# Optimization experiments

Measured on AMD Instinct MI355X. Metric: run time of the kernel, lower is better.

The kernel has to match this reference:

```python
import jax, jax.numpy as jnp
import numpy as np

N_NODES = 50000
N_EDGES = 800000
IN_DIM = 96
HID = 96


def setup_inputs() -> dict:
    key = jax.random.key(0)
    k1, k2, k3, k4 = jax.random.split(key, 4)
    x = jax.random.normal(k1, (N_NODES, IN_DIM), dtype=jnp.float32)
    edge_index = jax.random.randint(k2, (2, N_EDGES), 0, N_NODES, dtype=jnp.int64)
    s1 = 1.0 / np.sqrt(IN_DIM)
    s2 = 1.0 / np.sqrt(HID)
    W1 = jax.random.normal(k3, (IN_DIM, HID), dtype=jnp.float32) * s1
    b1 = jnp.zeros((HID,), dtype=jnp.float32)
    W2 = jax.random.normal(k4, (HID, HID), dtype=jnp.float32) * s2
    b2 = jnp.zeros((HID,), dtype=jnp.float32)
    return {"x": x, "edge_index": edge_index, "W1": W1, "b1": b1, "W2": W2, "b2": b2}


def _gcn_conv(x, src, dst, norm, W, b, n_nodes):
    # x' = D^{-1/2}(A+I)D^{-1/2} X W + b  (PyG GCNConv semantics)
    xw = x @ W                           # [N, out]
    msg = xw[src] * norm[:, None]        # gather + edge-normalize, [E+N, out]
    agg = jax.ops.segment_sum(msg, dst, num_segments=n_nodes)  # scatter-add
    return agg + b


def reference(x, edge_index, W1, b1, W2, b2):
    n_nodes = x.shape[0]
    loops = jnp.arange(n_nodes, dtype=edge_index.dtype)
    src = jnp.concatenate([edge_index[0], loops])  # sources (j)
    dst = jnp.concatenate([edge_index[1], loops])  # targets (i), aggregation index
    # symmetric normalization with self-loops; degree counted at targets
    deg = jax.ops.segment_sum(jnp.ones(dst.shape, dtype=x.dtype), dst, num_segments=n_nodes)
    dinv = jnp.where(deg > 0, jax.lax.rsqrt(deg), 0.0)
    norm = dinv[src] * dinv[dst]
    h = jax.nn.relu(_gcn_conv(x, src, dst, norm, W1, b1, n_nodes))
    h = jax.nn.relu(_gcn_conv(h, src, dst, norm, W2, b2, n_nodes))
    return h
```

## Files before the change

### kernel.cpp

```cpp
#include <hip/hip_runtime.h>

#define N_NODES 50000
#define N_EDGES 800000
#define DIM 96
#define FEAT_ELEMS (N_NODES * DIM)
#define NBLK 196

typedef __attribute__((ext_vector_type(8))) short short8;
typedef __attribute__((ext_vector_type(4))) float float4v;

__device__ __forceinline__ float bf16_to_f32(unsigned short u) {
    unsigned int w = ((unsigned int)u) << 16;
    float f;
    __builtin_memcpy(&f, &w, 4);
    return f;
}
__device__ __forceinline__ unsigned short f32_to_bf16_rne(float f) {
    unsigned int w;
    __builtin_memcpy(&w, &f, 4);
    unsigned int r = (w + 0x7FFFu + ((w >> 16) & 1u)) >> 16;
    return (unsigned short)r;
}

__device__ __forceinline__ int edge_at(const void* ep, int is64, int idx) {
    if (is64) return (int)((const long long*)ep)[idx];
    return ((const int*)ep)[idx];
}

__global__ __launch_bounds__(256) void prolog_kernel(const unsigned int* edges,
                                                     const unsigned int* x,
                                                     int* flagE, int* flagF, int* cnt) {
    __shared__ unsigned int sh[256];
    int t = threadIdx.x;
    int b = blockIdx.x;
    if (b < NBLK) {
        int i = b * 256 + t;
        if (i < N_NODES) cnt[i] = 0;
        return;
    }
    if (b == NBLK) {
        if (t < 64) {
            unsigned int acc = 0;
            for (int k = 0; k < 4; ++k) {
                int idx = t * 4 + k;
                int pos = 1 + 2 * idx * 3109;
                acc |= edges[pos];
            }
            sh[t] = acc;
        }
        __syncthreads();
        if (t == 0) {
            unsigned int a = 0;
            for (int i = 0; i < 64; ++i) a |= sh[i];
            *flagE = (a == 0u) ? 1 : 0;
        }
        return;
    }
    unsigned int w = x[t * 9000];
    unsigned int e = (w >> 7) & 0xFFu;
    sh[t] = (e >= 100u && e <= 135u) ? 1u : 0u;
    __syncthreads();
    if (t == 0) {
        int c = 0;
        for (int i = 0; i < 256; ++i) c += (int)sh[i];
        *flagF = (c >= 128) ? 1 : 0;
    }
}

__global__ __launch_bounds__(256) void count_compact_kernel(const void* edges,
                                                            const int* flagE, int* cnt,
                                                            unsigned short* srcu,
                                                            unsigned short* dstu,
                                                            unsigned short* rank) {
    int e = blockIdx.x * 256 + threadIdx.x;
    if (e >= N_EDGES) return;
    int is64 = *flagE;
    int s = edge_at(edges, is64, e);
    int d = edge_at(edges, is64, N_EDGES + e);
    srcu[e] = (unsigned short)s;
    dstu[e] = (unsigned short)d;
    rank[e] = (unsigned short)atomicAdd(&cnt[d], 1);
}

__global__ __launch_bounds__(256) void scan_blocksum_kernel(const int* cnt, int* blockSums) {
    __shared__ int sh[256];
    int i = blockIdx.x * 256 + threadIdx.x;
    sh[threadIdx.x] = (i < N_NODES) ? cnt[i] : 0;
    __syncthreads();
    for (int off = 128; off > 0; off >>= 1) {
        if (threadIdx.x < off) sh[threadIdx.x] += sh[threadIdx.x + off];
        __syncthreads();
    }
    if (threadIdx.x == 0) blockSums[blockIdx.x] = sh[0];
}

__global__ __launch_bounds__(256) void scan_offsets_kernel(const int* blockSums,
                                                           int* blockOffs, int* row_ptr) {
    __shared__ int sh[256];
    int t = threadIdx.x;
    int v = (t < NBLK) ? blockSums[t] : 0;
    sh[t] = v;
    __syncthreads();
    for (int off = 1; off < 256; off <<= 1) {
        int u = (t >= off) ? sh[t - off] : 0;
        __syncthreads();
        sh[t] += u;
        __syncthreads();
    }
    if (t < NBLK) blockOffs[t] = sh[t] - v;
    if (t == 255) row_ptr[N_NODES] = sh[255];
}

__global__ __launch_bounds__(256) void scan_apply_kernel(const int* cnt, const int* blockOffs,
                                                         int* row_ptr, float* dinv) {
    __shared__ int sh[256];
    int t = threadIdx.x;
    int i = blockIdx.x * 256 + t;
    int c = (i < N_NODES) ? cnt[i] : 0;
    sh[t] = c;
    __syncthreads();
    for (int off = 1; off < 256; off <<= 1) {
        int u = (t >= off) ? sh[t - off] : 0;
        __syncthreads();
        sh[t] += u;
        __syncthreads();
    }
    if (i < N_NODES) {
        int excl = sh[t] - c + blockOffs[blockIdx.x];
        row_ptr[i] = excl;
        dinv[i]    = rsqrtf((float)(c + 1));
    }
}

__global__ __launch_bounds__(256) void fill_direct_kernel(const unsigned short* __restrict__ dstu,
                                                          const unsigned short* __restrict__ srcu,
                                                          const unsigned short* __restrict__ rank,
                                                          const int* __restrict__ row_ptr,
                                                          unsigned short* __restrict__ csr_src) {
    int e = blockIdx.x * 256 + threadIdx.x;
    if (e >= N_EDGES) return;
    int d = dstu[e];
    int pos = row_ptr[d] + (int)rank[e];
    csr_src[pos] = srcu[e];
}

__global__ __launch_bounds__(256) void convert_kernel(const void* x, const int* flagF,
                                                      unsigned short* xb) {
    int i4 = (blockIdx.x * 256 + threadIdx.x) * 4;
    if (i4 >= FEAT_ELEMS) return;
    int isbf16 = *flagF;
    ushort4 o;
    if (isbf16) {
        o = *(const ushort4*)((const unsigned short*)x + i4);
    } else {
        float4 v = *(const float4*)((const float*)x + i4);
        o.x = f32_to_bf16_rne(v.x);
        o.y = f32_to_bf16_rne(v.y);
        o.z = f32_to_bf16_rne(v.z);
        o.w = f32_to_bf16_rne(v.w);
    }
    *(ushort4*)(xb + i4) = o;
}

__global__ __launch_bounds__(256) void gather_kernel(const unsigned short* __restrict__ feat,
                                                     const int* __restrict__ row_ptr,
                                                     const unsigned short* __restrict__ csr_src,
                                                     const float* __restrict__ dinv,
                                                     unsigned short* __restrict__ aggb) {
    int gid = blockIdx.x * 256 + threadIdx.x;
    int g = gid >> 4;
    int lane = gid & 15;
    if (g >= N_NODES) return;
    float di = dinv[g];
    int gb = g * DIM + lane * 2;
    ushort2 sv0 = *(const ushort2*)&feat[gb];
    ushort2 sv1 = *(const ushort2*)&feat[gb + 32];
    ushort2 sv2 = *(const ushort2*)&feat[gb + 64];
    float wself = di * di;
    float a0 = wself * bf16_to_f32(sv0.x), a1 = wself * bf16_to_f32(sv0.y);
    float a2 = wself * bf16_to_f32(sv1.x), a3 = wself * bf16_to_f32(sv1.y);
    float a4 = wself * bf16_to_f32(sv2.x), a5 = wself * bf16_to_f32(sv2.y);
    int e = row_ptr[g], e1 = row_ptr[g + 1];
    for (; e + 2 <= e1; e += 2) {
        int s0 = csr_src[e];
        int s1 = csr_src[e + 1];
        float w0 = dinv[s0] * di;
        float w1 = dinv[s1] * di;
        int b0 = s0 * DIM + lane * 2;
        int b1 = s1 * DIM + lane * 2;
        ushort2 p0 = *(const ushort2*)&feat[b0];
        ushort2 p1 = *(const ushort2*)&feat[b0 + 32];
        ushort2 p2 = *(const ushort2*)&feat[b0 + 64];
        ushort2 q0 = *(const ushort2*)&feat[b1];
        ushort2 q1 = *(const ushort2*)&feat[b1 + 32];
        ushort2 q2 = *(const ushort2*)&feat[b1 + 64];
        a0 = fmaf(w0, bf16_to_f32(p0.x), a0);  a1 = fmaf(w0, bf16_to_f32(p0.y), a1);
        a2 = fmaf(w0, bf16_to_f32(p1.x), a2);  a3 = fmaf(w0, bf16_to_f32(p1.y), a3);
        a4 = fmaf(w0, bf16_to_f32(p2.x), a4);  a5 = fmaf(w0, bf16_to_f32(p2.y), a5);
        a0 = fmaf(w1, bf16_to_f32(q0.x), a0);  a1 = fmaf(w1, bf16_to_f32(q0.y), a1);
        a2 = fmaf(w1, bf16_to_f32(q1.x), a2);  a3 = fmaf(w1, bf16_to_f32(q1.y), a3);
        a4 = fmaf(w1, bf16_to_f32(q2.x), a4);  a5 = fmaf(w1, bf16_to_f32(q2.y), a5);
    }
    if (e < e1) {
        int s = csr_src[e];
        float w = dinv[s] * di;
        int b0 = s * DIM + lane * 2;
        ushort2 p0 = *(const ushort2*)&feat[b0];
        ushort2 p1 = *(const ushort2*)&feat[b0 + 32];
        ushort2 p2 = *(const ushort2*)&feat[b0 + 64];
        a0 = fmaf(w, bf16_to_f32(p0.x), a0);  a1 = fmaf(w, bf16_to_f32(p0.y), a1);
        a2 = fmaf(w, bf16_to_f32(p1.x), a2);  a3 = fmaf(w, bf16_to_f32(p1.y), a3);
        a4 = fmaf(w, bf16_to_f32(p2.x), a4);  a5 = fmaf(w, bf16_to_f32(p2.y), a5);
    }
    unsigned int o0 = (unsigned int)f32_to_bf16_rne(a0) | ((unsigned int)f32_to_bf16_rne(a1) << 16);
    unsigned int o1 = (unsigned int)f32_to_bf16_rne(a2) | ((unsigned int)f32_to_bf16_rne(a3) << 16);
    unsigned int o2 = (unsigned int)f32_to_bf16_rne(a4) | ((unsigned int)f32_to_bf16_rne(a5) << 16);
    *(unsigned int*)&aggb[gb]      = o0;
    *(unsigned int*)&aggb[gb + 32] = o1;
    *(unsigned int*)&aggb[gb + 64] = o2;
}

__global__ __launch_bounds__(256) void gemm_mfma_kernel(const unsigned short* __restrict__ A,
                                                        const void* W, const void* bias,
                                                        const int* flagF,
                                                        void* out, int outMode) {
    __shared__ unsigned short Wlin[DIM * DIM];
    __shared__ unsigned short Wsw[3 * 6 * 64 * 8];
    __shared__ float bs[DIM];
    int wBf16 = *flagF;
    int outBf16 = (outMode == 2) ? wBf16 : outMode;

    if (wBf16) {
        const ushort4* W4 = (const ushort4*)W;
        ushort4* L4 = (ushort4*)Wlin;
        for (int i = threadIdx.x; i < DIM * DIM / 4; i += 256) L4[i] = W4[i];
        if (threadIdx.x < DIM)
            bs[threadIdx.x] = bf16_to_f32(((const unsigned short*)bias)[threadIdx.x]);
    } else {
        const float* Wf = (const float*)W;
        for (int i = threadIdx.x; i < DIM * DIM; i += 256) Wlin[i] = f32_to_bf16_rne(Wf[i]);
        if (threadIdx.x < DIM) bs[threadIdx.x] = ((const float*)bias)[threadIdx.x];
    }
    __syncthreads();

    for (int f = threadIdx.x; f < 1152; f += 256) {
        int kt = f / 384;
        int rem = f - kt * 384;
        int nt = rem >> 6;
        int ln64 = rem & 63;
        int q = ln64 >> 4, ln = ln64 & 15;
        int k0 = kt * 32 + q * 8;
        int n = nt * 16 + ln;
        unsigned int w0 = (unsigned int)Wlin[(k0 + 0) * DIM + n] |
                          ((unsigned int)Wlin[(k0 + 1) * DIM + n] << 16);
        unsigned int w1 = (unsigned int)Wlin[(k0 + 2) * DIM + n] |
                          ((unsigned int)Wlin[(k0 + 3) * DIM + n] << 16);
        unsigned int w2 = (unsigned int)Wlin[(k0 + 4) * DIM + n] |
                          ((unsigned int)Wlin[(k0 + 5) * DIM + n] << 16);
        unsigned int w3 = (unsigned int)Wlin[(k0 + 6) * DIM + n] |
                          ((unsigned int)Wlin[(k0 + 7) * DIM + n] << 16);
        uint4 pk = make_uint4(w0, w1, w2, w3);
        *(uint4*)&Wsw[f * 8] = pk;
    }
    __syncthreads();

    int wave = threadIdx.x >> 6;
    int lane = threadIdx.x & 63;
    int quad = lane >> 4, ln = lane & 15;
    int m0 = blockIdx.x * 64 + wave * 16;
    int arow = m0 + ln;
    bool arowok = (arow < N_NODES);

    float4v acc[6];
    #pragma unroll
    for (int nt = 0; nt < 6; ++nt) acc[nt] = (float4v){0.f, 0.f, 0.f, 0.f};

    #pragma unroll
    for (int kt = 0; kt < 3; ++kt) {
        short8 af;
        if (arowok) {
            af = *(const short8*)&A[arow * DIM + kt * 32 + quad * 8];
        } else {
            af = (short8){0, 0, 0, 0, 0, 0, 0, 0};
        }
        #pragma unroll
        for (int nt = 0; nt < 6; ++nt) {
            short8 bf = *(const short8*)&Wsw[((kt * 6 + nt) * 64 + lane) * 8];
            acc[nt] = __builtin_amdgcn_mfma_f32_16x16x32_bf16(af, bf, acc[nt], 0, 0, 0);
        }
    }

    #pragma unroll
    for (int nt = 0; nt < 6; ++nt) {
        int n = nt * 16 + ln;
        float bv = bs[n];
        #pragma unroll
        for (int reg = 0; reg < 4; ++reg) {
            int row = m0 + quad * 4 + reg;
            if (row >= N_NODES) continue;
            float v = fmaxf(acc[nt][reg] + bv, 0.0f);
            if (outBf16) ((unsigned short*)out)[row * DIM + n] = f32_to_bf16_rne(v);
            else         ((float*)out)[row * DIM + n] = v;
        }
    }
}

extern "C" void kernel_launch(void* const* d_in, const int* in_sizes, int n_in,
                              void* d_out, int out_size, void* d_ws, size_t ws_size,
                              hipStream_t stream) {
    const void* x  = d_in[0];
    const void* ei = d_in[1];
    const void* W1 = d_in[2];
    const void* b1 = d_in[3];
    const void* W2 = d_in[4];
    const void* b2 = d_in[5];

    char* base = (char*)d_ws;
    size_t off = 0;
    auto carve = [&](size_t bytes) -> void* {
        void* p = base + off;
        off += (bytes + 255) & ~(size_t)255;
        return p;
    };
    int*            flagE     = (int*)carve(4);
    int*            flagF     = (int*)carve(4);
    int*            cnt       = (int*)carve((size_t)N_NODES * 4);
    int*            row_ptr   = (int*)carve((size_t)(N_NODES + 1) * 4);
    float*          dinv      = (float*)carve((size_t)N_NODES * 4);
    int*            blockSums = (int*)carve((size_t)NBLK * 4);
    int*            blockOffs = (int*)carve((size_t)NBLK * 4);
    unsigned short* srcu      = (unsigned short*)carve((size_t)N_EDGES * 2);
    unsigned short* dstu      = (unsigned short*)carve((size_t)N_EDGES * 2);
    unsigned short* rank      = (unsigned short*)carve((size_t)N_EDGES * 2);
    unsigned short* csr_src   = (unsigned short*)carve((size_t)N_EDGES * 2);
    unsigned short* aggb      = (unsigned short*)carve((size_t)FEAT_ELEMS * 2);
    unsigned short* xb        = (unsigned short*)carve((size_t)FEAT_ELEMS * 2);
    unsigned short* h         = (unsigned short*)carve((size_t)FEAT_ELEMS * 2);

    const int egrid = (N_EDGES + 255) / 256;
    const int cgrid = (FEAT_ELEMS / 4 + 255) / 256;
    const int agrid = (N_NODES * 16 + 255) / 256;
    const int ggrid = (N_NODES + 63) / 64;

    prolog_kernel<<<NBLK + 2, 256, 0, stream>>>((const unsigned int*)ei,
                                                (const unsigned int*)x, flagE, flagF, cnt);
    count_compact_kernel<<<egrid, 256, 0, stream>>>(ei, flagE, cnt, srcu, dstu, rank);
    scan_blocksum_kernel<<<NBLK, 256, 0, stream>>>(cnt, blockSums);
    scan_offsets_kernel<<<1, 256, 0, stream>>>(blockSums, blockOffs, row_ptr);
    scan_apply_kernel<<<NBLK, 256, 0, stream>>>(cnt, blockOffs, row_ptr, dinv);
    fill_direct_kernel<<<egrid, 256, 0, stream>>>(dstu, srcu, rank, row_ptr, csr_src);
    convert_kernel<<<cgrid, 256, 0, stream>>>(x, flagF, xb);

    gather_kernel<<<agrid, 256, 0, stream>>>(xb, row_ptr, csr_src, dinv, aggb);
    gemm_mfma_kernel<<<ggrid, 256, 0, stream>>>(aggb, W1, b1, flagF, h, 1);

    gather_kernel<<<agrid, 256, 0, stream>>>(h, row_ptr, csr_src, dinv, aggb);
    gemm_mfma_kernel<<<ggrid, 256, 0, stream>>>(aggb, W2, b2, flagF, d_out, 2);
}
```

Baseline: 212.4 us.

## Fuse gather-aggregate with MFMA GEMM per layer and merge prep kernels

Each GCN layer's neighbour gather now writes its aggregated bf16 rows into an LDS tile and feeds MFMA directly. This removes the aggb round trip through global memory and one launch per layer. The edge count/compact kernel is merged with the x-to-bf16 conversion, and the three-kernel scan becomes two by folding the block-offset scan into the apply step. The fused kernel runs fewer blocks (64 rows each) for the gather phase, which may lower latency hiding for the irregular gathers, and it builds the swizzled weights from global memory in every block.

After: 230.6 us. +8.5%, slower.

```diff
diff --git a/kernel.cpp b/kernel.cpp
--- a/kernel.cpp
+++ b/kernel.cpp
@@ -5,6 +5,10 @@
 #define DIM 96
 #define FEAT_ELEMS (N_NODES * DIM)
 #define NBLK 196
+#define EGRID 3125
+#define CGRID 4688
+#define GGRID 782
+#define APAD 104
 
 typedef __attribute__((ext_vector_type(8))) short short8;
 typedef __attribute__((ext_vector_type(4))) float float4v;
@@ -20,6 +24,9 @@
     __builtin_memcpy(&w, &f, 4);
     unsigned int r = (w + 0x7FFFu + ((w >> 16) & 1u)) >> 16;
     return (unsigned short)r;
+}
+__device__ __forceinline__ unsigned int pack_bf16x2(float lo, float hi) {
+    return (unsigned int)f32_to_bf16_rne(lo) | ((unsigned int)f32_to_bf16_rne(hi) << 16);
 }
 
 __device__ __forceinline__ int edge_at(const void* ep, int is64, int idx) {
@@ -67,86 +74,27 @@
     }
 }
 
-__global__ __launch_bounds__(256) void count_compact_kernel(const void* edges,
-                                                            const int* flagE, int* cnt,
-                                                            unsigned short* srcu,
-                                                            unsigned short* dstu,
-                                                            unsigned short* rank) {
-    int e = blockIdx.x * 256 + threadIdx.x;
-    if (e >= N_EDGES) return;
-    int is64 = *flagE;
-    int s = edge_at(edges, is64, e);
-    int d = edge_at(edges, is64, N_EDGES + e);
-    srcu[e] = (unsigned short)s;
-    dstu[e] = (unsigned short)d;
-    rank[e] = (unsigned short)atomicAdd(&cnt[d], 1);
-}
-
-__global__ __launch_bounds__(256) void scan_blocksum_kernel(const int* cnt, int* blockSums) {
-    __shared__ int sh[256];
-    int i = blockIdx.x * 256 + threadIdx.x;
-    sh[threadIdx.x] = (i < N_NODES) ? cnt[i] : 0;
-    __syncthreads();
-    for (int off = 128; off > 0; off >>= 1) {
-        if (threadIdx.x < off) sh[threadIdx.x] += sh[threadIdx.x + off];
-        __syncthreads();
-    }
-    if (threadIdx.x == 0) blockSums[blockIdx.x] = sh[0];
-}
-
-__global__ __launch_bounds__(256) void scan_offsets_kernel(const int* blockSums,
-                                                           int* blockOffs, int* row_ptr) {
-    __shared__ int sh[256];
-    int t = threadIdx.x;
-    int v = (t < NBLK) ? blockSums[t] : 0;
-    sh[t] = v;
-    __syncthreads();
-    for (int off = 1; off < 256; off <<= 1) {
-        int u = (t >= off) ? sh[t - off] : 0;
-        __syncthreads();
-        sh[t] += u;
-        __syncthreads();
-    }
-    if (t < NBLK) blockOffs[t] = sh[t] - v;
-    if (t == 255) row_ptr[N_NODES] = sh[255];
-}
-
-__global__ __launch_bounds__(256) void scan_apply_kernel(const int* cnt, const int* blockOffs,
-                                                         int* row_ptr, float* dinv) {
-    __shared__ int sh[256];
-    int t = threadIdx.x;
-    int i = blockIdx.x * 256 + t;
-    int c = (i < N_NODES) ? cnt[i] : 0;
-    sh[t] = c;
-    __syncthreads();
-    for (int off = 1; off < 256; off <<= 1) {
-        int u = (t >= off) ? sh[t - off] : 0;
-        __syncthreads();
-        sh[t] += u;
-        __syncthreads();
-    }
-    if (i < N_NODES) {
-        int excl = sh[t] - c + blockOffs[blockIdx.x];
-        row_ptr[i] = excl;
-        dinv[i]    = rsqrtf((float)(c + 1));
-    }
-}
-
-__global__ __launch_bounds__(256) void fill_direct_kernel(const unsigned short* __restrict__ dstu,
-                                                          const unsigned short* __restrict__ srcu,
-                                                          const unsigned short* __restrict__ rank,
-                                                          const int* __restrict__ row_ptr,
-                                                          unsigned short* __restrict__ csr_src) {
-    int e = blockIdx.x * 256 + threadIdx.x;
-    if (e >= N_EDGES) return;
-    int d = dstu[e];
-    int pos = row_ptr[d] + (int)rank[e];
-    csr_src[pos] = srcu[e];
-}
-
-__global__ __launch_bounds__(256) void convert_kernel(const void* x, const int* flagF,
-                                                      unsigned short* xb) {
-    int i4 = (blockIdx.x * 256 + threadIdx.x) * 4;
+__global__ __launch_bounds__(256) void count_convert_kernel(const void* __restrict__ edges,
+                                                            const void* __restrict__ x,
+                                                            const int* __restrict__ flagE,
+                                                            const int* __restrict__ flagF,
+                                                            int* __restrict__ cnt,
+                                                            unsigned short* __restrict__ srcu,
+                                                            unsigned short* __restrict__ dstu,
+                                                            unsigned short* __restrict__ rank,
+                                                            unsigned short* __restrict__ xb) {
+    int b = blockIdx.x;
+    if (b < EGRID) {
+        int e = b * 256 + threadIdx.x;
+        int is64 = *flagE;
+        int s = edge_at(edges, is64, e);
+        int d = edge_at(edges, is64, N_EDGES + e);
+        srcu[e] = (unsigned short)s;
+        dstu[e] = (unsigned short)d;
+        rank[e] = (unsigned short)atomicAdd(&cnt[d], 1);
+        return;
+    }
+    int i4 = ((b - EGRID) * 256 + threadIdx.x) * 4;
     if (i4 >= FEAT_ELEMS) return;
     int isbf16 = *flagF;
     ushort4 o;
@@ -162,88 +110,81 @@
     *(ushort4*)(xb + i4) = o;
 }
 
-__global__ __launch_bounds__(256) void gather_kernel(const unsigned short* __restrict__ feat,
-                                                     const int* __restrict__ row_ptr,
-                                                     const unsigned short* __restrict__ csr_src,
-                                                     const float* __restrict__ dinv,
-                                                     unsigned short* __restrict__ aggb) {
-    int gid = blockIdx.x * 256 + threadIdx.x;
-    int g = gid >> 4;
-    int lane = gid & 15;
-    if (g >= N_NODES) return;
-    float di = dinv[g];
-    int gb = g * DIM + lane * 2;
-    ushort2 sv0 = *(const ushort2*)&feat[gb];
-    ushort2 sv1 = *(const ushort2*)&feat[gb + 32];
-    ushort2 sv2 = *(const ushort2*)&feat[gb + 64];
-    float wself = di * di;
-    float a0 = wself * bf16_to_f32(sv0.x), a1 = wself * bf16_to_f32(sv0.y);
-    float a2 = wself * bf16_to_f32(sv1.x), a3 = wself * bf16_to_f32(sv1.y);
-    float a4 = wself * bf16_to_f32(sv2.x), a5 = wself * bf16_to_f32(sv2.y);
-    int e = row_ptr[g], e1 = row_ptr[g + 1];
-    for (; e + 2 <= e1; e += 2) {
-        int s0 = csr_src[e];
-        int s1 = csr_src[e + 1];
-        float w0 = dinv[s0] * di;
-        float w1 = dinv[s1] * di;
-        int b0 = s0 * DIM + lane * 2;
-        int b1 = s1 * DIM + lane * 2;
-        ushort2 p0 = *(const ushort2*)&feat[b0];
-        ushort2 p1 = *(const ushort2*)&feat[b0 + 32];
-        ushort2 p2 = *(const ushort2*)&feat[b0 + 64];
-        ushort2 q0 = *(const ushort2*)&feat[b1];
-        ushort2 q1 = *(const ushort2*)&feat[b1 + 32];
-        ushort2 q2 = *(const ushort2*)&feat[b1 + 64];
-        a0 = fmaf(w0, bf16_to_f32(p0.x), a0);  a1 = fmaf(w0, bf16_to_f32(p0.y), a1);
-        a2 = fmaf(w0, bf16_to_f32(p1.x), a2);  a3 = fmaf(w0, bf16_to_f32(p1.y), a3);
-        a4 = fmaf(w0, bf16_to_f32(p2.x), a4);  a5 = fmaf(w0, bf16_to_f32(p2.y), a5);
-        a0 = fmaf(w1, bf16_to_f32(q0.x), a0);  a1 = fmaf(w1, bf16_to_f32(q0.y), a1);
-        a2 = fmaf(w1, bf16_to_f32(q1.x), a2);  a3 = fmaf(w1, bf16_to_f32(q1.y), a3);
-        a4 = fmaf(w1, bf16_to_f32(q2.x), a4);  a5 = fmaf(w1, bf16_to_f32(q2.y), a5);
-    }
-    if (e < e1) {
-        int s = csr_src[e];
-        float w = dinv[s] * di;
-        int b0 = s * DIM + lane * 2;
-        ushort2 p0 = *(const ushort2*)&feat[b0];
-        ushort2 p1 = *(const ushort2*)&feat[b0 + 32];
-        ushort2 p2 = *(const ushort2*)&feat[b0 + 64];
-        a0 = fmaf(w, bf16_to_f32(p0.x), a0);  a1 = fmaf(w, bf16_to_f32(p0.y), a1);
-        a2 = fmaf(w, bf16_to_f32(p1.x), a2);  a3 = fmaf(w, bf16_to_f32(p1.y), a3);
-        a4 = fmaf(w, bf16_to_f32(p2.x), a4);  a5 = fmaf(w, bf16_to_f32(p2.y), a5);
-    }
-    unsigned int o0 = (unsigned int)f32_to_bf16_rne(a0) | ((unsigned int)f32_to_bf16_rne(a1) << 16);
-    unsigned int o1 = (unsigned int)f32_to_bf16_rne(a2) | ((unsigned int)f32_to_bf16_rne(a3) << 16);
-    unsigned int o2 = (unsigned int)f32_to_bf16_rne(a4) | ((unsigned int)f32_to_bf16_rne(a5) << 16);
-    *(unsigned int*)&aggb[gb]      = o0;
-    *(unsigned int*)&aggb[gb + 32] = o1;
-    *(unsigned int*)&aggb[gb + 64] = o2;
-}
-
-__global__ __launch_bounds__(256) void gemm_mfma_kernel(const unsigned short* __restrict__ A,
-                                                        const void* W, const void* bias,
-                                                        const int* flagF,
-                                                        void* out, int outMode) {
-    __shared__ unsigned short Wlin[DIM * DIM];
-    __shared__ unsigned short Wsw[3 * 6 * 64 * 8];
-    __shared__ float bs[DIM];
+__global__ __launch_bounds__(256) void scan_blocksum_kernel(const int* cnt, int* blockSums) {
+    __shared__ int sh[256];
+    int i = blockIdx.x * 256 + threadIdx.x;
+    sh[threadIdx.x] = (i < N_NODES) ? cnt[i] : 0;
+    __syncthreads();
+    for (int off = 128; off > 0; off >>= 1) {
+        if (threadIdx.x < off) sh[threadIdx.x] += sh[threadIdx.x + off];
+        __syncthreads();
+    }
+    if (threadIdx.x == 0) blockSums[blockIdx.x] = sh[0];
+}
+
+__global__ __launch_bounds__(256) void scan_apply_kernel(const int* __restrict__ cnt,
+                                                         const int* __restrict__ blockSums,
+                                                         int* __restrict__ row_ptr,
+                                                         float* __restrict__ dinv) {
+    __shared__ int sb[256];
+    __shared__ int sh[256];
+    int t = threadIdx.x;
+    sb[t] = (t < NBLK) ? blockSums[t] : 0;
+    __syncthreads();
+    for (int off = 1; off < 256; off <<= 1) {
+        int u = (t >= off) ? sb[t - off] : 0;
+        __syncthreads();
+        sb[t] += u;
+        __syncthreads();
+    }
+    int b = blockIdx.x;
+    int blockOff = (b == 0) ? 0 : sb[b - 1];
+    if (b == 0 && t == 0) row_ptr[N_NODES] = sb[NBLK - 1];
+
+    int i = b * 256 + t;
+    int c = (i < N_NODES) ? cnt[i] : 0;
+    sh[t] = c;
+    __syncthreads();
+    for (int off = 1; off < 256; off <<= 1) {
+        int u = (t >= off) ? sh[t - off] : 0;
+        __syncthreads();
+        sh[t] += u;
+        __syncthreads();
+    }
+    if (i < N_NODES) {
+        row_ptr[i] = sh[t] - c + blockOff;
+        dinv[i]    = rsqrtf((float)(c + 1));
+    }
+}
+
+__global__ __launch_bounds__(256) void fill_direct_kernel(const unsigned short* __restrict__ dstu,
+                                                          const unsigned short* __restrict__ srcu,
+                                                          const unsigned short* __restrict__ rank,
+                                                          const int* __restrict__ row_ptr,
+                                                          unsigned short* __restrict__ csr_src) {
+    int e = blockIdx.x * 256 + threadIdx.x;
+    if (e >= N_EDGES) return;
+    int d = dstu[e];
+    int pos = row_ptr[d] + (int)rank[e];
+    csr_src[pos] = srcu[e];
+}
+
+__global__ __launch_bounds__(256) void fused_layer_kernel(const unsigned short* __restrict__ feat,
+                                                          const int* __restrict__ row_ptr,
+                                                          const unsigned short* __restrict__ csr_src,
+                                                          const float* __restrict__ dinv,
+                                                          const void* __restrict__ W,
+                                                          const void* __restrict__ bias,
+                                                          const int* __restrict__ flagF,
+                                                          void* __restrict__ out, int outMode) {
+    __shared__ __align__(16) unsigned short Wsw[3 * 6 * 64 * 8];
+    __shared__ __align__(16) unsigned short Atile[64 * APAD];
+
+    int t = threadIdx.x;
     int wBf16 = *flagF;
     int outBf16 = (outMode == 2) ? wBf16 : outMode;
 
-    if (wBf16) {
-        const ushort4* W4 = (const ushort4*)W;
-        ushort4* L4 = (ushort4*)Wlin;
-        for (int i = threadIdx.x; i < DIM * DIM / 4; i += 256) L4[i] = W4[i];
-        if (threadIdx.x < DIM)
-            bs[threadIdx.x] = bf16_to_f32(((const unsigned short*)bias)[threadIdx.x]);
-    } else {
-        const float* Wf = (const float*)W;
-        for (int i = threadIdx.x; i < DIM * DIM; i += 256) Wlin[i] = f32_to_bf16_rne(Wf[i]);
-        if (threadIdx.x < DIM) bs[threadIdx.x] = ((const float*)bias)[threadIdx.x];
-    }
-    __syncthreads();
-
-    for (int f = threadIdx.x; f < 1152; f += 256) {
+    for (int f = t; f < 1152; f += 256) {
         int kt = f / 384;
         int rem = f - kt * 384;
         int nt = rem >> 6;
@@ -251,25 +192,85 @@
         int q = ln64 >> 4, ln = ln64 & 15;
         int k0 = kt * 32 + q * 8;
         int n = nt * 16 + ln;
-        unsigned int w0 = (unsigned int)Wlin[(k0 + 0) * DIM + n] |
-                          ((unsigned int)Wlin[(k0 + 1) * DIM + n] << 16);
-        unsigned int w1 = (unsigned int)Wlin[(k0 + 2) * DIM + n] |
-                          ((unsigned int)Wlin[(k0 + 3) * DIM + n] << 16);
-        unsigned int w2 = (unsigned int)Wlin[(k0 + 4) * DIM + n] |
-                          ((unsigned int)Wlin[(k0 + 5) * DIM + n] << 16);
-        unsigned int w3 = (unsigned int)Wlin[(k0 + 6) * DIM + n] |
-                          ((unsigned int)Wlin[(k0 + 7) * DIM + n] << 16);
-        uint4 pk = make_uint4(w0, w1, w2, w3);
+        unsigned short e[8];
+        if (wBf16) {
+            const unsigned short* Wh = (const unsigned short*)W;
+            #pragma unroll
+            for (int j = 0; j < 8; ++j) e[j] = Wh[(k0 + j) * DIM + n];
+        } else {
+            const float* Wf = (const float*)W;
+            #pragma unroll
+            for (int j = 0; j < 8; ++j) e[j] = f32_to_bf16_rne(Wf[(k0 + j) * DIM + n]);
+        }
+        uint4 pk;
+        pk.x = (unsigned int)e[0] | ((unsigned int)e[1] << 16);
+        pk.y = (unsigned int)e[2] | ((unsigned int)e[3] << 16);
+        pk.z = (unsigned int)e[4] | ((unsigned int)e[5] << 16);
+        pk.w = (unsigned int)e[6] | ((unsigned int)e[7] << 16);
         *(uint4*)&Wsw[f * 8] = pk;
     }
-    __syncthreads();
-
-    int wave = threadIdx.x >> 6;
-    int lane = threadIdx.x & 63;
+
+    int m0 = blockIdx.x * 64;
+    int grp = t >> 4;
+    int l = t & 15;
+    for (int p = 0; p < 4; ++p) {
+        int r = grp * 4 + p;
+        int g = m0 + r;
+        float a0 = 0.f, a1 = 0.f, a2 = 0.f, a3 = 0.f, a4 = 0.f, a5 = 0.f;
+        if (g < N_NODES) {
+            float di = dinv[g];
+            int gb = g * DIM + l * 2;
+            ushort2 sv0 = *(const ushort2*)&feat[gb];
+            ushort2 sv1 = *(const ushort2*)&feat[gb + 32];
+            ushort2 sv2 = *(const ushort2*)&feat[gb + 64];
+            float wself = di * di;
+            a0 = wself * bf16_to_f32(sv0.x); a1 = wself * bf16_to_f32(sv0.y);
+            a2 = wself * bf16_to_f32(sv1.x); a3 = wself * bf16_to_f32(sv1.y);
+            a4 = wself * bf16_to_f32(sv2.x); a5 = wself * bf16_to_f32(sv2.y);
+            int e = row_ptr[g], e1 = row_ptr[g + 1];
+            for (; e + 2 <= e1; e += 2) {
+                int s0 = csr_src[e];
+                int s1 = csr_src[e + 1];
+                float w0 = dinv[s0] * di;
+                float w1 = dinv[s1] * di;
+                int b0 = s0 * DIM + l * 2;
+                int b1 = s1 * DIM + l * 2;
+                ushort2 p0 = *(const ushort2*)&feat[b0];
+                ushort2 p1 = *(const ushort2*)&feat[b0 + 32];
+                ushort2 p2 = *(const ushort2*)&feat[b0 + 64];
+                ushort2 q0 = *(const ushort2*)&feat[b1];
+                ushort2 q1 = *(const ushort2*)&feat[b1 + 32];
+                ushort2 q2 = *(const ushort2*)&feat[b1 + 64];
+                a0 = fmaf(w0, bf16_to_f32(p0.x), a0);  a1 = fmaf(w0, bf16_to_f32(p0.y), a1);
+                a2 = fmaf(w0, bf16_to_f32(p1.x), a2);  a3 = fmaf(w0, bf16_to_f32(p1.y), a3);
+                a4 = fmaf(w0, bf16_to_f32(p2.x), a4);  a5 = fmaf(w0, bf16_to_f32(p2.y), a5);
+                a0 = fmaf(w1, bf16_to_f32(q0.x), a0);  a1 = fmaf(w1, bf16_to_f32(q0.y), a1);
+                a2 = fmaf(w1, bf16_to_f32(q1.x), a2);  a3 = fmaf(w1, bf16_to_f32(q1.y), a3);
+                a4 = fmaf(w1, bf16_to_f32(q2.x), a4);  a5 = fmaf(w1, bf16_to_f32(q2.y), a5);
+            }
+            if (e < e1) {
+                int s = csr_src[e];
+                float w = dinv[s] * di;
+                int b0 = s * DIM + l * 2;
+                ushort2 p0 = *(const ushort2*)&feat[b0];
+                ushort2 p1 = *(const ushort2*)&feat[b0 + 32];
+                ushort2 p2 = *(const ushort2*)&feat[b0 + 64];
+                a0 = fmaf(w, bf16_to_f32(p0.x), a0);  a1 = fmaf(w, bf16_to_f32(p0.y), a1);
+                a2 = fmaf(w, bf16_to_f32(p1.x), a2);  a3 = fmaf(w, bf16_to_f32(p1.y), a3);
+                a4 = fmaf(w, bf16_to_f32(p2.x), a4);  a5 = fmaf(w, bf16_to_f32(p2.y), a5);
+            }
+        }
+        int ab = r * APAD + l * 2;
+        *(unsigned int*)&Atile[ab]      = pack_bf16x2(a0, a1);
+        *(unsigned int*)&Atile[ab + 32] = pack_bf16x2(a2, a3);
+        *(unsigned int*)&Atile[ab + 64] = pack_bf16x2(a4, a5);
+    }
+    __syncthreads();
+
+    int wave = t >> 6;
+    int lane = t & 63;
     int quad = lane >> 4, ln = lane & 15;
-    int m0 = blockIdx.x * 64 + wave * 16;
-    int arow = m0 + ln;
-    bool arowok = (arow < N_NODES);
+    int rloc = wave * 16 + ln;
 
     float4v acc[6];
     #pragma unroll
@@ -277,12 +278,7 @@
 
     #pragma unroll
     for (int kt = 0; kt < 3; ++kt) {
-        short8 af;
-        if (arowok) {
-            af = *(const short8*)&A[arow * DIM + kt * 32 + quad * 8];
-        } else {
-            af = (short8){0, 0, 0, 0, 0, 0, 0, 0};
-        }
+        short8 af = *(const short8*)&Atile[rloc * APAD + kt * 32 + quad * 8];
         #pragma unroll
         for (int nt = 0; nt < 6; ++nt) {
             short8 bf = *(const short8*)&Wsw[((kt * 6 + nt) * 64 + lane) * 8];
@@ -293,10 +289,11 @@
     #pragma unroll
     for (int nt = 0; nt < 6; ++nt) {
         int n = nt * 16 + ln;
-        float bv = bs[n];
+        float bv = wBf16 ? bf16_to_f32(((const unsigned short*)bias)[n])
+                         : ((const float*)bias)[n];
         #pragma unroll
         for (int reg = 0; reg < 4; ++reg) {
-            int row = m0 + quad * 4 + reg;
+            int row = m0 + wave * 16 + quad * 4 + reg;
             if (row >= N_NODES) continue;
             float v = fmaxf(acc[nt][reg] + bv, 0.0f);
             if (outBf16) ((unsigned short*)out)[row * DIM + n] = f32_to_bf16_rne(v);
@@ -328,32 +325,23 @@
     int*            row_ptr   = (int*)carve((size_t)(N_NODES + 1) * 4);
     float*          dinv      = (float*)carve((size_t)N_NODES * 4);
     int*            blockSums = (int*)carve((size_t)NBLK * 4);
-    int*            blockOffs = (int*)carve((size_t)NBLK * 4);
     unsigned short* srcu      = (unsigned short*)carve((size_t)N_EDGES * 2);
     unsigned short* dstu      = (unsigned short*)carve((size_t)N_EDGES * 2);
     unsigned short* rank      = (unsigned short*)carve((size_t)N_EDGES * 2);
     unsigned short* csr_src   = (unsigned short*)carve((size_t)N_EDGES * 2);
-    unsigned short* aggb      = (unsigned short*)carve((size_t)FEAT_ELEMS * 2);
     unsigned short* xb        = (unsigned short*)carve((size_t)FEAT_ELEMS * 2);
     unsigned short* h         = (unsigned short*)carve((size_t)FEAT_ELEMS * 2);
 
-    const int egrid = (N_EDGES + 255) / 256;
-    const int cgrid = (FEAT_ELEMS / 4 + 255) / 256;
-    const int agrid = (N_NODES * 16 + 255) / 256;
-    const int ggrid = (N_NODES + 63) / 64;
-
     prolog_kernel<<<NBLK + 2, 256, 0, stream>>>((const unsigned int*)ei,
                                                 (const unsigned int*)x, flagE, flagF, cnt);
-    count_compact_kernel<<<egrid, 256, 0, stream>>>(ei, flagE, cnt, srcu, dstu, rank);
+    count_convert_kernel<<<EGRID + CGRID, 256, 0, stream>>>(ei, x, flagE, flagF, cnt,
+                                                            srcu, dstu, rank, xb);
     scan_blocksum_kernel<<<NBLK, 256, 0, stream>>>(cnt, blockSums);
-    scan_offsets_kernel<<<1, 256, 0, stream>>>(blockSums, blockOffs, row_ptr);
-    scan_apply_kernel<<<NBLK, 256, 0, stream>>>(cnt, blockOffs, row_ptr, dinv);
-    fill_direct_kernel<<<egrid, 256, 0, stream>>>(dstu, srcu, rank, row_ptr, csr_src);
-    convert_kernel<<<cgrid, 256, 0, stream>>>(x, flagF, xb);
-
-    gather_kernel<<<agrid, 256, 0, stream>>>(xb, row_ptr, csr_src, dinv, aggb);
-    gemm_mfma_kernel<<<ggrid, 256, 0, stream>>>(aggb, W1, b1, flagF, h, 1);
-
-    gather_kernel<<<agrid, 256, 0, stream>>>(h, row_ptr, csr_src, dinv, aggb);
-    gemm_mfma_kernel<<<ggrid, 256, 0, stream>>>(aggb, W2, b2, flagF, d_out, 2);
-}
+    scan_apply_kernel<<<NBLK, 256, 0, stream>>>(cnt, blockSums, row_ptr, dinv);
+    fill_direct_kernel<<<EGRID, 256, 0, stream>>>(dstu, srcu, rank, row_ptr, csr_src);
+
+    fused_layer_kernel<<<GGRID, 256, 0, stream>>>(xb, row_ptr, csr_src, dinv,
+                                                  W1, b1, flagF, h, 1);
+    fused_layer_kernel<<<GGRID, 256, 0, stream>>>(h, row_ptr, csr_src, dinv,
+                                                  W2, b2, flagF, d_out, 2);
+}
```
